# Kernel tuning notes

Measured on AMD Instinct MI355X. Metric: run time of the kernel, lower is better.

The kernel has to match this reference:

```python
import math
import jax, jax.numpy as jnp
import numpy as np

NUM_HEADS = 16
HEAD_DIM = 64
NB_FEATURES = 256
EPS = 1e-06
DATA_NORM = HEAD_DIM ** (-0.25)


def setup_inputs() -> dict:
    key = jax.random.key(0)
    ks = jax.random.split(key, 5)
    B, N, C = 4, 4096, 1024
    x = jax.random.normal(ks[0], (B, N, C), dtype=jnp.float32)
    w_qkv = jax.random.normal(ks[1], (C, 3 * C), dtype=jnp.float32) * (C ** -0.5)
    b_qkv = jnp.zeros((3 * C,), dtype=jnp.float32)
    w_out = jax.random.normal(ks[2], (C, C), dtype=jnp.float32) * (C ** -0.5)
    b_out = jnp.zeros((C,), dtype=jnp.float32)
    proj = jax.random.normal(ks[3], (NUM_HEADS, NB_FEATURES, HEAD_DIM), dtype=jnp.float32)
    proj = proj / jnp.linalg.norm(proj, axis=-1, keepdims=True)  # F.normalize(dim=-1)
    return {"x": x, "w_qkv": w_qkv, "b_qkv": b_qkv, "w_out": w_out, "b_out": b_out,
            "proj_matrix": proj}


def _feature_map(x, proj):
    # x: [b,h,n,d], proj: [h,m,d] -> [b,h,n,m]
    x = x * DATA_NORM
    x_proj = jnp.einsum('bhnd,hmd->bhnm', x, proj)
    sq_norms = 0.5 * jnp.sum(x * x, axis=-1, keepdims=True)
    x_proj = x_proj - sq_norms
    x_proj = x_proj - jnp.max(x_proj, axis=-1, keepdims=True)
    return (jnp.exp(x_proj) + EPS) / math.sqrt(NB_FEATURES)


def reference(x, w_qkv, b_qkv, w_out, b_out, proj_matrix):
    B, N, C = x.shape
    h, d = NUM_HEADS, HEAD_DIM
    qkv = x @ w_qkv + b_qkv                     # [B,N,3C]
    q, k, v = jnp.split(qkv, 3, axis=-1)
    to_heads = lambda z: z.reshape(B, N, h, d).transpose(0, 2, 1, 3)  # [B,h,N,d]
    q, k, v = to_heads(q), to_heads(k), to_heads(v)

    q_prime = _feature_map(q, proj_matrix)      # [B,h,N,m]
    k_prime = _feature_map(k, proj_matrix)      # [B,h,N,m]

    k_sum = jnp.sum(k_prime, axis=2)                          # [B,h,m]
    kv = jnp.einsum('bhnm,bhnd->bhmd', k_prime, v)            # [B,h,m,d]
    numerator = jnp.einsum('bhnm,bhmd->bhnd', q_prime, kv)    # [B,h,N,d]
    denominator = jnp.einsum('bhnm,bhm->bhn', q_prime, k_sum) + EPS
    out = numerator / denominator[..., None]

    out = out.transpose(0, 2, 1, 3).reshape(B, N, C)
    return out @ w_out + b_out
```

## Files before the change

kernel.cpp:

```cpp
#include <hip/hip_runtime.h>
#include <hip/hip_bf16.h>
#include <stdint.h>


#define DN 0.35355339059327379f
#define EPSF 1e-6f
#define INV_SQRT_M 0.0625f

typedef __attribute__((ext_vector_type(8))) short bf16x8;
typedef __attribute__((ext_vector_type(4))) float f32x4;

static __device__ __forceinline__ short f2bf(float f) {
    __hip_bfloat16 h = __float2bfloat16(f);
    return *(short*)&h;
}
static __device__ __forceinline__ void gload16(const void* g, void* l) {
    __builtin_amdgcn_global_load_lds(
        (const __attribute__((address_space(1))) void*)g,
        (__attribute__((address_space(3))) void*)l,
        16, 0, 0);
}

__global__ __launch_bounds__(256) void conv_x(const float* __restrict__ X,
                                              short* __restrict__ Xb) {
    int i = blockIdx.x * 256 + threadIdx.x;
    float4 v = ((const float4*)X)[i];
    short4 o;
    o.x = f2bf(v.x); o.y = f2bf(v.y); o.z = f2bf(v.z); o.w = f2bf(v.w);
    ((short4*)Xb)[i] = o;
}

__global__ __launch_bounds__(256) void convt_w(const float* __restrict__ W,
                                               short* __restrict__ WT,
                                               int K, int NN) {
    __shared__ short tile[64][66];
    int t = threadIdx.x;
    int k0 = blockIdx.y * 64, n0 = blockIdx.x * 64;
    for (int i = t; i < 4096; i += 256) {
        int r = i >> 6, c = i & 63;
        tile[r][c] = f2bf(W[(size_t)(k0 + r) * NN + n0 + c]);
    }
    __syncthreads();
    for (int i = t; i < 4096; i += 256) {
        int r = i >> 6, c = i & 63;
        WT[(size_t)(n0 + r) * K + k0 + c] = tile[c][r];
    }
}

__global__ __launch_bounds__(256) void conv_proj(const float* __restrict__ proj,
                                                 short* __restrict__ pjb) {
    int e = blockIdx.x * 256 + threadIdx.x;
    int m = (e >> 6) & 255, d = e & 63;
    int base = e & ~63;
    pjb[base + (d ^ ((m & 7) << 3))] = f2bf(proj[e]);
}

__global__ __launch_bounds__(256) void mfma_gemm_qkv(const short* __restrict__ A,
                                                     const short* __restrict__ BT,
                                                     const float* __restrict__ bias,
                                                     short* __restrict__ Qh,
                                                     short* __restrict__ Kh,
                                                     short* __restrict__ Vt) {
    const int K = 1024;
    __shared__ short lA[128 * 32];
    __shared__ short lB[128 * 32];
    int t = threadIdx.x, lane = t & 63, w = t >> 6;
    int wm = w >> 1, wn = w & 1;
    int rowBase = blockIdx.y * 128, colBase = blockIdx.x * 128;

    int rs = (lane >> 2), cb = (lane & 3) * 16;
    const char* gA0 = (const char*)(A + (size_t)(rowBase + w * 32 + rs) * K) + cb;
    const char* gA1 = (const char*)(A + (size_t)(rowBase + w * 32 + 16 + rs) * K) + cb;
    const char* gB0 = (const char*)(BT + (size_t)(colBase + w * 32 + rs) * K) + cb;
    const char* gB1 = (const char*)(BT + (size_t)(colBase + w * 32 + 16 + rs) * K) + cb;
    char* dA0 = (char*)lA + (w * 32) * 64;
    char* dA1 = (char*)lA + (w * 32 + 16) * 64;
    char* dB0 = (char*)lB + (w * 32) * 64;
    char* dB1 = (char*)lB + (w * 32 + 16) * 64;

    int offA[4], offB[4];
#pragma unroll
    for (int m = 0; m < 4; ++m) {
        offA[m] = (wm * 64 + m * 16 + (lane & 15)) * 64 + (lane >> 4) * 16;
        offB[m] = (wn * 64 + m * 16 + (lane & 15)) * 64 + (lane >> 4) * 16;
    }

    f32x4 acc[4][4];
#pragma unroll
    for (int m = 0; m < 4; ++m)
#pragma unroll
        for (int n = 0; n < 4; ++n) acc[m][n] = (f32x4){0.f, 0.f, 0.f, 0.f};

    for (int k0 = 0; k0 < K; k0 += 32) {
        size_t kb = (size_t)k0 * 2;
        gload16(gA0 + kb, dA0);
        gload16(gA1 + kb, dA1);
        gload16(gB0 + kb, dB0);
        gload16(gB1 + kb, dB1);
        __syncthreads();
        bf16x8 af[4], bfr[4];
#pragma unroll
        for (int m = 0; m < 4; ++m) af[m] = *(const bf16x8*)((const char*)lA + offA[m]);
#pragma unroll
        for (int n = 0; n < 4; ++n) bfr[n] = *(const bf16x8*)((const char*)lB + offB[n]);
#pragma unroll
        for (int m = 0; m < 4; ++m)
#pragma unroll
            for (int n = 0; n < 4; ++n)
                acc[m][n] = __builtin_amdgcn_mfma_f32_16x16x32_bf16(af[m], bfr[n], acc[m][n], 0, 0, 0);
        __syncthreads();
    }

    int li = lane & 15, g = lane >> 4;
    float bcol[4];
#pragma unroll
    for (int n = 0; n < 4; ++n)
        bcol[n] = bias[colBase + wn * 64 + n * 16 + li];
#pragma unroll
    for (int n = 0; n < 4; ++n) {
        int gc = colBase + wn * 64 + n * 16 + li;
        int which = gc >> 10, cc = gc & 1023, hh = cc >> 6, dd = cc & 63;
        if (which == 2) {
#pragma unroll
            for (int m = 0; m < 4; ++m) {
                int gr0 = rowBase + wm * 64 + m * 16 + g * 4;
                int b = gr0 >> 12, nn0 = gr0 & 4095;
                short4 o;
                o.x = f2bf(acc[m][n][0] + bcol[n]);
                o.y = f2bf(acc[m][n][1] + bcol[n]);
                o.z = f2bf(acc[m][n][2] + bcol[n]);
                o.w = f2bf(acc[m][n][3] + bcol[n]);
                int nsw = (nn0 & ~63) | ((nn0 & 63) ^ ((dd & 7) << 3));
                *(short4*)&Vt[((size_t)(b * 16 + hh) * 64 + dd) * 4096 + nsw] = o;
            }
        } else {
            short* dst = (which == 0) ? Qh : Kh;
#pragma unroll
            for (int m = 0; m < 4; ++m) {
#pragma unroll
                for (int j = 0; j < 4; ++j) {
                    int gr = rowBase + wm * 64 + m * 16 + g * 4 + j;
                    int b = gr >> 12, nn = gr & 4095;
                    int dsw = dd ^ ((nn & 7) << 3);
                    dst[((size_t)(b * 16 + hh) * 4096 + nn) * 64 + dsw] =
                        f2bf((acc[m][n][j] + bcol[n]) * DN);
                }
            }
        }
    }
}

__global__ __launch_bounds__(256) void mfma_gemm_out(const short* __restrict__ A,
                                                     const short* __restrict__ BT,
                                                     const float* __restrict__ bias,
                                                     float* __restrict__ C) {
    const int K = 1024, NN = 1024;
    __shared__ short lA[128 * 32];
    __shared__ short lB[128 * 32];
    int t = threadIdx.x, lane = t & 63, w = t >> 6;
    int wm = w >> 1, wn = w & 1;
    int rowBase = blockIdx.y * 128, colBase = blockIdx.x * 128;

    int rs = (lane >> 2), cb = (lane & 3) * 16;
    const char* gA0 = (const char*)(A + (size_t)(rowBase + w * 32 + rs) * K) + cb;
    const char* gA1 = (const char*)(A + (size_t)(rowBase + w * 32 + 16 + rs) * K) + cb;
    const char* gB0 = (const char*)(BT + (size_t)(colBase + w * 32 + rs) * K) + cb;
    const char* gB1 = (const char*)(BT + (size_t)(colBase + w * 32 + 16 + rs) * K) + cb;
    char* dA0 = (char*)lA + (w * 32) * 64;
    char* dA1 = (char*)lA + (w * 32 + 16) * 64;
    char* dB0 = (char*)lB + (w * 32) * 64;
    char* dB1 = (char*)lB + (w * 32 + 16) * 64;

    int offA[4], offB[4];
#pragma unroll
    for (int m = 0; m < 4; ++m) {
        offA[m] = (wm * 64 + m * 16 + (lane & 15)) * 64 + (lane >> 4) * 16;
        offB[m] = (wn * 64 + m * 16 + (lane & 15)) * 64 + (lane >> 4) * 16;
    }

    f32x4 acc[4][4];
#pragma unroll
    for (int m = 0; m < 4; ++m)
#pragma unroll
        for (int n = 0; n < 4; ++n) acc[m][n] = (f32x4){0.f, 0.f, 0.f, 0.f};

    for (int k0 = 0; k0 < K; k0 += 32) {
        size_t kb = (size_t)k0 * 2;
        gload16(gA0 + kb, dA0);
        gload16(gA1 + kb, dA1);
        gload16(gB0 + kb, dB0);
        gload16(gB1 + kb, dB1);
        __syncthreads();
        bf16x8 af[4], bfr[4];
#pragma unroll
        for (int m = 0; m < 4; ++m) af[m] = *(const bf16x8*)((const char*)lA + offA[m]);
#pragma unroll
        for (int n = 0; n < 4; ++n) bfr[n] = *(const bf16x8*)((const char*)lB + offB[n]);
#pragma unroll
        for (int m = 0; m < 4; ++m)
#pragma unroll
            for (int n = 0; n < 4; ++n)
                acc[m][n] = __builtin_amdgcn_mfma_f32_16x16x32_bf16(af[m], bfr[n], acc[m][n], 0, 0, 0);
        __syncthreads();
    }

    float bcol[4];
#pragma unroll
    for (int n = 0; n < 4; ++n)
        bcol[n] = bias[colBase + wn * 64 + n * 16 + (lane & 15)];
#pragma unroll
    for (int m = 0; m < 4; ++m) {
#pragma unroll
        for (int j = 0; j < 4; ++j) {
            int gr = rowBase + wm * 64 + m * 16 + (lane >> 4) * 4 + j;
#pragma unroll
            for (int n = 0; n < 4; ++n) {
                int gc = colBase + wn * 64 + n * 16 + (lane & 15);
                C[(size_t)gr * NN + gc] = acc[m][n][j] + bcol[n];
            }
        }
    }
}

__global__ __launch_bounds__(256) void fmap_mfma(const short* __restrict__ Kh,
                                                 const short* __restrict__ Vt,
                                                 const short* __restrict__ pjb,
                                                 float* __restrict__ kvpart,
                                                 float* __restrict__ kspart) {
    int bh = blockIdx.y, ch = blockIdx.x, h = bh & 15;
    int t = threadIdx.x, lane = t & 63, w = t >> 6;
    int g = lane >> 4, li = lane & 15;
    __shared__ __align__(16) short pj[256 * 64];
    __shared__ __align__(16) short kt[64 * 64];
    __shared__ __align__(16) short vt[64 * 64];
    __shared__ __align__(16) short Pl[4][64 * 40];
    __shared__ __align__(16) float maxw[4][64];

    {
        const short* psrc = pjb + (size_t)h * 16384;
#pragma unroll
        for (int c2 = 0; c2 < 8; ++c2) {
            int c = 8 * w + c2;
            gload16(psrc + c * 512 + lane * 8, pj + c * 512);
        }
    }

    f32x4 acc[4][4];
#pragma unroll
    for (int i = 0; i < 4; ++i)
#pragma unroll
        for (int j = 0; j < 4; ++j) acc[i][j] = (f32x4){0.f, 0.f, 0.f, 0.f};
    float ksacc[4] = {0.f, 0.f, 0.f, 0.f};

    const short* kbase = Kh + ((size_t)bh * 4096 + ch * 512) * 64;
    const short* vbase = Vt + (size_t)bh * 64 * 4096 + ch * 512;
    int swz = (li & 7) << 4;

    for (int tile = 0; tile < 8; ++tile) {
        __syncthreads();
#pragma unroll
        for (int c2 = 0; c2 < 2; ++c2) {
            int c = 2 * w + c2;
            gload16(kbase + (size_t)(tile * 64) * 64 + c * 512 + lane * 8,
                    kt + c * 512);
            int d = 8 * c + (lane >> 3);
            gload16(vbase + (size_t)d * 4096 + tile * 64 + (lane & 7) * 8,
                    vt + c * 512);
        }
        __syncthreads();

        f32x4 sacc[4][4];
#pragma unroll
        for (int i = 0; i < 4; ++i)
#pragma unroll
            for (int j = 0; j < 4; ++j) sacc[i][j] = (f32x4){0.f, 0.f, 0.f, 0.f};
#pragma unroll
        for (int ks = 0; ks < 2; ++ks) {
            int kb = ks * 64 + g * 16;
            bf16x8 afr[4], bfr[4];
#pragma unroll
            for (int ni = 0; ni < 4; ++ni)
                afr[ni] = *(const bf16x8*)((const char*)kt +
                           (16 * ni + li) * 128 + (kb ^ swz));
#pragma unroll
            for (int mi = 0; mi < 4; ++mi)
                bfr[mi] = *(const bf16x8*)((const char*)pj +
                           (64 * w + 16 * mi + li) * 128 + (kb ^ swz));
#pragma unroll
            for (int ni = 0; ni < 4; ++ni)
#pragma unroll
                for (int mi = 0; mi < 4; ++mi)
                    sacc[ni][mi] = __builtin_amdgcn_mfma_f32_16x16x32_bf16(
                        afr[ni], bfr[mi], sacc[ni][mi], 0, 0, 0);
        }

        float mxl[4][4];
#pragma unroll
        for (int ni = 0; ni < 4; ++ni)
#pragma unroll
            for (int jj = 0; jj < 4; ++jj) {
                float m0 = fmaxf(sacc[ni][0][jj], sacc[ni][1][jj]);
                float m1 = fmaxf(sacc[ni][2][jj], sacc[ni][3][jj]);
                mxl[ni][jj] = fmaxf(m0, m1);
            }
#pragma unroll
        for (int off = 1; off <= 8; off <<= 1)
#pragma unroll
            for (int ni = 0; ni < 4; ++ni)
#pragma unroll
                for (int jj = 0; jj < 4; ++jj)
                    mxl[ni][jj] = fmaxf(mxl[ni][jj], __shfl_xor(mxl[ni][jj], off));
        if (li == 0) {
#pragma unroll
            for (int ni = 0; ni < 4; ++ni)
                *(float4*)&maxw[w][16 * ni + 4 * g] =
                    make_float4(mxl[ni][0], mxl[ni][1], mxl[ni][2], mxl[ni][3]);
        }
        __syncthreads();

#pragma unroll
        for (int hf = 0; hf < 2; ++hf) {
#pragma unroll
            for (int ni2 = 0; ni2 < 2; ++ni2) {
                int ni = 2 * hf + ni2;
                float4 a0 = *(const float4*)&maxw[0][16 * ni + 4 * g];
                float4 a1 = *(const float4*)&maxw[1][16 * ni + 4 * g];
                float4 a2 = *(const float4*)&maxw[2][16 * ni + 4 * g];
                float4 a3 = *(const float4*)&maxw[3][16 * ni + 4 * g];
                float mm[4];
                mm[0] = fmaxf(fmaxf(a0.x, a1.x), fmaxf(a2.x, a3.x));
                mm[1] = fmaxf(fmaxf(a0.y, a1.y), fmaxf(a2.y, a3.y));
                mm[2] = fmaxf(fmaxf(a0.z, a1.z), fmaxf(a2.z, a3.z));
                mm[3] = fmaxf(fmaxf(a0.w, a1.w), fmaxf(a2.w, a3.w));
#pragma unroll
                for (int mi = 0; mi < 4; ++mi) {
                    float p0 = (__expf(sacc[ni][mi][0] - mm[0]) + EPSF) * INV_SQRT_M;
                    float p1 = (__expf(sacc[ni][mi][1] - mm[1]) + EPSF) * INV_SQRT_M;
                    float p2 = (__expf(sacc[ni][mi][2] - mm[2]) + EPSF) * INV_SQRT_M;
                    float p3 = (__expf(sacc[ni][mi][3] - mm[3]) + EPSF) * INV_SQRT_M;
                    ksacc[mi] += (p0 + p1) + (p2 + p3);
                    uint32_t u0 = (uint32_t)(uint16_t)f2bf(p0) |
                                  ((uint32_t)(uint16_t)f2bf(p1) << 16);
                    uint32_t u1 = (uint32_t)(uint16_t)f2bf(p2) |
                                  ((uint32_t)(uint16_t)f2bf(p3) << 16);
                    int m_l = 16 * mi + li;
                    *(uint2*)((char*)Pl[w] + m_l * 80 + 32 * ni2 + 8 * g) =
                        make_uint2(u0, u1);
                }
            }
#pragma unroll
            for (int mi = 0; mi < 4; ++mi) {
                bf16x8 pa = *(const bf16x8*)((const char*)Pl[w] +
                             (16 * mi + li) * 80 + 16 * g);
#pragma unroll
                for (int di = 0; di < 4; ++di) {
                    bf16x8 bv = *(const bf16x8*)((const char*)vt +
                                 (16 * di + li) * 128 + ((64 * hf + 16 * g) ^ swz));
                    acc[mi][di] = __builtin_amdgcn_mfma_f32_16x16x32_bf16(
                        pa, bv, acc[mi][di], 0, 0, 0);
                }
            }
        }
    }

#pragma unroll
    for (int mi = 0; mi < 4; ++mi) {
        ksacc[mi] += __shfl_xor(ksacc[mi], 16);
        ksacc[mi] += __shfl_xor(ksacc[mi], 32);
    }
    if (lane < 16) {
#pragma unroll
        for (int mi = 0; mi < 4; ++mi)
            kspart[(bh * 8 + ch) * 256 + 64 * w + 16 * mi + li] = ksacc[mi];
    }
    float* kvb = kvpart + (size_t)(bh * 8 + ch) * 16384;
#pragma unroll
    for (int mi = 0; mi < 4; ++mi)
#pragma unroll
        for (int di = 0; di < 4; ++di) {
            int d = 16 * di + li, m0 = 64 * w + 16 * mi + 4 * g;
            *(float4*)&kvb[d * 256 + m0] =
                make_float4(acc[mi][di][0], acc[mi][di][1],
                            acc[mi][di][2], acc[mi][di][3]);
        }
}

__global__ __launch_bounds__(256) void reduce_kv(const float* __restrict__ kvpart,
                                                 const float* __restrict__ kspart,
                                                 short* __restrict__ kvsT) {
    int bh = blockIdx.y, bx = blockIdx.x, t = threadIdx.x;
    if (bx < 4) {
#pragma unroll
        for (int i = 0; i < 16; ++i) {
            int idx = t + i * 256;
            int d = 16 * bx + (idx >> 8), m = idx & 255;
            float s = 0.f;
            size_t base = ((size_t)(bh * 8) * 64 + d) * 256 + m;
#pragma unroll
            for (int c = 0; c < 8; ++c) s += kvpart[base + (size_t)c * 16384];
            int widx = (m & 128) + ((m & 127) ^ ((d & 7) << 3));
            kvsT[((size_t)bh * 80 + d) * 256 + widx] = f2bf(s);
        }
    } else {
        float s = 0.f;
#pragma unroll
        for (int c = 0; c < 8; ++c) s += kspart[((bh * 8 + c) << 8) + t];
        kvsT[((size_t)bh * 80 + 64) * 256 + t] = f2bf(s);
        for (int i = t; i < 15 * 256; i += 256) {
            int r = 65 + (i >> 8), cc = i & 255;
            kvsT[((size_t)bh * 80 + r) * 256 + cc] = 0;
        }
    }
}

__global__ __launch_bounds__(256) void contract_mfma(
        const short* __restrict__ Qh,
        const short* __restrict__ pjb,
        const short* __restrict__ kvsT,
        short* __restrict__ attn) {
    int bh = blockIdx.y, rb = blockIdx.x, h = bh & 15, b = bh >> 4;
    int t = threadIdx.x, lane = t & 63, w = t >> 6;
    __shared__ __align__(16) short qs[64 * 64];
    __shared__ __align__(16) short pj[128 * 64];
    __shared__ __align__(16) short Pl[64 * 128];
    __shared__ __align__(16) short kvl[80 * 128];

    {
        const short* src = Qh + ((size_t)bh * 4096 + rb * 64) * 64;
#pragma unroll
        for (int c2 = 0; c2 < 2; ++c2) {
            int c = 2 * w + c2;
            gload16(src + (c * 8 + (lane >> 3)) * 64 + (lane & 7) * 8,
                    qs + c * 512);
        }
    }

    f32x4 acc5[5];
#pragma unroll
    for (int i = 0; i < 5; ++i) acc5[i] = (f32x4){0.f, 0.f, 0.f, 0.f};

    int g = lane >> 4, li = lane & 15;

    for (int half = 0; half < 2; ++half) {
        __syncthreads();
        const short* psrc = pjb + (size_t)h * 16384 + half * 8192;
#pragma unroll
        for (int c2 = 0; c2 < 4; ++c2) {
            int c = 4 * w + c2;
            gload16(psrc + (c * 8 + (lane >> 3)) * 64 + (lane & 7) * 8,
                    pj + c * 512);
        }
        const short* ksrc = kvsT + (size_t)bh * 80 * 256 + half * 128;
#pragma unroll
        for (int c2 = 0; c2 < 5; ++c2) {
            int c = 5 * w + c2;
            gload16(ksrc + (c * 4 + (lane >> 4)) * 256 + (lane & 15) * 8,
                    kvl + c * 512);
        }
        __syncthreads();

        f32x4 sacc[2][4];
#pragma unroll
        for (int mi = 0; mi < 2; ++mi)
#pragma unroll
            for (int ni = 0; ni < 4; ++ni) sacc[mi][ni] = (f32x4){0.f, 0.f, 0.f, 0.f};
#pragma unroll
        for (int ks = 0; ks < 2; ++ks) {
            int kbyte = ks * 64 + g * 16;
            bf16x8 afr[2], bfr[4];
#pragma unroll
            for (int mi = 0; mi < 2; ++mi) {
                int mr = 32 * w + 16 * mi + li;
                afr[mi] = *(const bf16x8*)((const char*)pj +
                           mr * 128 + (kbyte ^ ((mr & 7) << 4)));
            }
#pragma unroll
            for (int ni = 0; ni < 4; ++ni) {
                int qr = 16 * ni + li;
                bfr[ni] = *(const bf16x8*)((const char*)qs +
                           qr * 128 + (kbyte ^ ((qr & 7) << 4)));
            }
#pragma unroll
            for (int mi = 0; mi < 2; ++mi)
#pragma unroll
                for (int ni = 0; ni < 4; ++ni)
                    sacc[mi][ni] = __builtin_amdgcn_mfma_f32_16x16x32_bf16(
                        afr[mi], bfr[ni], sacc[mi][ni], 0, 0, 0);
        }

#pragma unroll
        for (int mi = 0; mi < 2; ++mi) {
            int m0 = 32 * w + 16 * mi + 4 * g;
#pragma unroll
            for (int ni = 0; ni < 4; ++ni) {
                int row = 16 * ni + li;
                float e0 = (__expf(sacc[mi][ni][0]) + EPSF) * INV_SQRT_M;
                float e1 = (__expf(sacc[mi][ni][1]) + EPSF) * INV_SQRT_M;
                float e2 = (__expf(sacc[mi][ni][2]) + EPSF) * INV_SQRT_M;
                float e3 = (__expf(sacc[mi][ni][3]) + EPSF) * INV_SQRT_M;
                uint32_t u0 = (uint32_t)(uint16_t)f2bf(e0) |
                              ((uint32_t)(uint16_t)f2bf(e1) << 16);
                uint32_t u1 = (uint32_t)(uint16_t)f2bf(e2) |
                              ((uint32_t)(uint16_t)f2bf(e3) << 16);
                int byte = row * 256 + ((m0 * 2) ^ ((row & 7) << 4));
                *(uint2*)((char*)Pl + byte) = make_uint2(u0, u1);
            }
        }
        __syncthreads();

        int rowA = 16 * w + li;
        int abase = rowA * 256;
        int asw = (rowA & 7) << 4;
#pragma unroll
        for (int ks = 0; ks < 4; ++ks) {
            int kbyte = ks * 64 + g * 16;
            bf16x8 pa = *(const bf16x8*)((const char*)Pl + abase + (kbyte ^ asw));
#pragma unroll
            for (int ni = 0; ni < 5; ++ni) {
                int rowB = 16 * ni + li;
                bf16x8 bv = *(const bf16x8*)((const char*)kvl +
                             rowB * 256 + (kbyte ^ ((rowB & 7) << 4)));
                acc5[ni] = __builtin_amdgcn_mfma_f32_16x16x32_bf16(
                    pa, bv, acc5[ni], 0, 0, 0);
            }
        }
    }

    float dj[4];
#pragma unroll
    for (int jj = 0; jj < 4; ++jj)
        dj[jj] = __shfl(acc5[4][jj], lane & 48) + EPSF;
#pragma unroll
    for (int ni = 0; ni < 4; ++ni) {
        int d = 16 * ni + li;
#pragma unroll
        for (int jj = 0; jj < 4; ++jj) {
            int n = rb * 64 + 16 * w + 4 * g + jj;
            attn[((size_t)b * 4096 + n) * 1024 + h * 64 + d] =
                f2bf(acc5[ni][jj] / dj[jj]);
        }
    }
}

extern "C" void kernel_launch(void* const* d_in, const int* in_sizes, int n_in,
                              void* d_out, int out_size, void* d_ws, size_t ws_size,
                              hipStream_t stream) {
    const float* x      = (const float*)d_in[0];
    const float* w_qkv  = (const float*)d_in[1];
    const float* b_qkv  = (const float*)d_in[2];
    const float* w_out  = (const float*)d_in[3];
    const float* b_out  = (const float*)d_in[4];
    const float* proj   = (const float*)d_in[5];
    float* out = (float*)d_out;

    char* w = (char*)d_ws;
    short* xb     = (short*)(w);
    short* wqT    = (short*)(w + 33554432);
    short* wOT    = (short*)(w + 39845888);
    short* Qh     = (short*)(w + 41943040);
    short* Kh     = (short*)(w + 75497472);
    short* Vt     = (short*)(w + 109051904);
    float* kvpart = (float*)(w);
    float* kspart = (float*)(w + 142606336);
    short* kvsT   = (short*)(w + 143130624);
    short* pjb    = (short*)(w + 145752064);
    short* attn   = Kh;

    conv_x<<<dim3(16384), 256, 0, stream>>>(x, xb);
    convt_w<<<dim3(48, 16), 256, 0, stream>>>(w_qkv, wqT, 1024, 3072);
    convt_w<<<dim3(16, 16), 256, 0, stream>>>(w_out, wOT, 1024, 1024);
    conv_proj<<<dim3(1024), 256, 0, stream>>>(proj, pjb);
    mfma_gemm_qkv<<<dim3(24, 128), 256, 0, stream>>>(xb, wqT, b_qkv, Qh, Kh, Vt);
    fmap_mfma<<<dim3(8, 64), 256, 0, stream>>>(Kh, Vt, pjb, kvpart, kspart);
    reduce_kv<<<dim3(5, 64), 256, 0, stream>>>(kvpart, kspart, kvsT);
    contract_mfma<<<dim3(64, 64), 256, 0, stream>>>(Qh, pjb, kvsT, attn);
    mfma_gemm_out<<<dim3(8, 128), 256, 0, stream>>>(attn, wOT, b_out, out);
}
```

Baseline: 341.6 us.

## Double-buffer GEMM K-loop with swizzled LDS, block remapping, and staged epilogue stores

Both projection GEMMs now share one core that stages 64-wide K tiles into two LDS buffers with an XOR swizzle. The next tile's loads are issued before computing the current one, so fewer barriers are needed and global latency overlaps the MFMA work. The 1D grid is remapped so neighbouring blocks share operand rows and columns for better L2 reuse. Epilogues stage results through LDS so Q/K and the output are written with wide vector stores instead of scattered scalar ones, at the cost of 64KB LDS per block, which may limit occupancy.

```diff
diff --git a/kernel.cpp b/kernel.cpp
--- a/kernel.cpp
+++ b/kernel.cpp
@@ -55,72 +55,105 @@
     pjb[base + (d ^ ((m & 7) << 3))] = f2bf(proj[e]);
 }
 
-__global__ __launch_bounds__(256) void mfma_gemm_qkv(const short* __restrict__ A,
-                                                     const short* __restrict__ BT,
-                                                     const float* __restrict__ bias,
-                                                     short* __restrict__ Qh,
-                                                     short* __restrict__ Kh,
-                                                     short* __restrict__ Vt) {
+__device__ __forceinline__ void gemm_core128(const short* __restrict__ A,
+                                             const short* __restrict__ BT,
+                                             int rowBase, int colBase,
+                                             char* smem, f32x4 acc[4][4]) {
     const int K = 1024;
-    __shared__ short lA[128 * 32];
-    __shared__ short lB[128 * 32];
     int t = threadIdx.x, lane = t & 63, w = t >> 6;
+    int li = lane & 15, g = lane >> 4;
     int wm = w >> 1, wn = w & 1;
-    int rowBase = blockIdx.y * 128, colBase = blockIdx.x * 128;
-
-    int rs = (lane >> 2), cb = (lane & 3) * 16;
-    const char* gA0 = (const char*)(A + (size_t)(rowBase + w * 32 + rs) * K) + cb;
-    const char* gA1 = (const char*)(A + (size_t)(rowBase + w * 32 + 16 + rs) * K) + cb;
-    const char* gB0 = (const char*)(BT + (size_t)(colBase + w * 32 + rs) * K) + cb;
-    const char* gB1 = (const char*)(BT + (size_t)(colBase + w * 32 + 16 + rs) * K) + cb;
-    char* dA0 = (char*)lA + (w * 32) * 64;
-    char* dA1 = (char*)lA + (w * 32 + 16) * 64;
-    char* dB0 = (char*)lB + (w * 32) * 64;
-    char* dB1 = (char*)lB + (w * 32 + 16) * 64;
-
-    int offA[4], offB[4];
-#pragma unroll
-    for (int m = 0; m < 4; ++m) {
-        offA[m] = (wm * 64 + m * 16 + (lane & 15)) * 64 + (lane >> 4) * 16;
-        offB[m] = (wn * 64 + m * 16 + (lane & 15)) * 64 + (lane >> 4) * 16;
-    }
+
+    const char* aSrc[4]; const char* bSrc[4]; int aOff[4];
+#pragma unroll
+    for (int c = 0; c < 4; ++c) {
+        int idx = c * 256 + t;
+        int r = idx >> 3, s = t & 7;
+        aOff[c] = idx * 16;
+        aSrc[c] = (const char*)(A + (size_t)(rowBase + r) * K + ((s ^ (r & 7)) * 8));
+        bSrc[c] = (const char*)(BT + (size_t)(colBase + r) * K + ((s ^ (r & 7)) * 8));
+    }
+#pragma unroll
+    for (int m = 0; m < 4; ++m)
+#pragma unroll
+        for (int n = 0; n < 4; ++n) acc[m][n] = (f32x4){0.f, 0.f, 0.f, 0.f};
+
+#pragma unroll
+    for (int c = 0; c < 4; ++c) {
+        gload16(aSrc[c], smem + aOff[c]);
+        gload16(bSrc[c], smem + 16384 + aOff[c]);
+    }
+
+    int swz = (li & 7) << 4;
+
+    for (int tt = 0; tt < 16; ++tt) {
+        int cur = tt & 1;
+        if (tt < 15) {
+            char* d = smem + (cur ^ 1) * 32768;
+#pragma unroll
+            for (int c = 0; c < 4; ++c) {
+                gload16(aSrc[c] + (size_t)(tt + 1) * 128, d + aOff[c]);
+                gload16(bSrc[c] + (size_t)(tt + 1) * 128, d + 16384 + aOff[c]);
+            }
+            asm volatile("s_waitcnt vmcnt(8)" ::: "memory");
+        } else {
+            asm volatile("s_waitcnt vmcnt(0)" ::: "memory");
+        }
+        __builtin_amdgcn_sched_barrier(0);
+        __builtin_amdgcn_s_barrier();
+        __builtin_amdgcn_sched_barrier(0);
+        __builtin_amdgcn_s_setprio(1);
+        const char* bA = smem + cur * 32768;
+        const char* bB = bA + 16384;
+#pragma unroll
+        for (int ks = 0; ks < 2; ++ks) {
+            int kb = ks * 64 + g * 16;
+            bf16x8 af[4], bv[4];
+#pragma unroll
+            for (int m = 0; m < 4; ++m)
+                af[m] = *(const bf16x8*)(bA + (wm * 64 + m * 16 + li) * 128 + (kb ^ swz));
+#pragma unroll
+            for (int n = 0; n < 4; ++n)
+                bv[n] = *(const bf16x8*)(bB + (wn * 64 + n * 16 + li) * 128 + (kb ^ swz));
+#pragma unroll
+            for (int m = 0; m < 4; ++m)
+#pragma unroll
+                for (int n = 0; n < 4; ++n)
+                    acc[m][n] = __builtin_amdgcn_mfma_f32_16x16x32_bf16(
+                        af[m], bv[n], acc[m][n], 0, 0, 0);
+        }
+        __builtin_amdgcn_s_setprio(0);
+        __builtin_amdgcn_sched_barrier(0);
+        __builtin_amdgcn_s_barrier();
+        __builtin_amdgcn_sched_barrier(0);
+    }
+}
+
+__global__ __launch_bounds__(256, 2) void mfma_gemm_qkv(
+        const short* __restrict__ A, const short* __restrict__ BT,
+        const float* __restrict__ bias,
+        short* __restrict__ Qh, short* __restrict__ Kh, short* __restrict__ Vt) {
+    __shared__ __align__(16) char smem[65536];
+    int t = threadIdx.x, lane = t & 63, w = t >> 6;
+    int li = lane & 15, g = lane >> 4, wm = w >> 1, wn = w & 1;
+    int lin = blockIdx.x;
+    int sz = (lin & 7) * 384 + (lin >> 3);
+    int bx = sz % 24, by = sz / 24;
+    int rowBase = by * 128, colBase = bx * 128;
 
     f32x4 acc[4][4];
-#pragma unroll
-    for (int m = 0; m < 4; ++m)
-#pragma unroll
-        for (int n = 0; n < 4; ++n) acc[m][n] = (f32x4){0.f, 0.f, 0.f, 0.f};
-
-    for (int k0 = 0; k0 < K; k0 += 32) {
-        size_t kb = (size_t)k0 * 2;
-        gload16(gA0 + kb, dA0);
-        gload16(gA1 + kb, dA1);
-        gload16(gB0 + kb, dB0);
-        gload16(gB1 + kb, dB1);
-        __syncthreads();
-        bf16x8 af[4], bfr[4];
-#pragma unroll
-        for (int m = 0; m < 4; ++m) af[m] = *(const bf16x8*)((const char*)lA + offA[m]);
-#pragma unroll
-        for (int n = 0; n < 4; ++n) bfr[n] = *(const bf16x8*)((const char*)lB + offB[n]);
-#pragma unroll
-        for (int m = 0; m < 4; ++m)
-#pragma unroll
-            for (int n = 0; n < 4; ++n)
-                acc[m][n] = __builtin_amdgcn_mfma_f32_16x16x32_bf16(af[m], bfr[n], acc[m][n], 0, 0, 0);
-        __syncthreads();
-    }
-
-    int li = lane & 15, g = lane >> 4;
+    gemm_core128(A, BT, rowBase, colBase, smem, acc);
+
     float bcol[4];
 #pragma unroll
-    for (int n = 0; n < 4; ++n)
-        bcol[n] = bias[colBase + wn * 64 + n * 16 + li];
-#pragma unroll
-    for (int n = 0; n < 4; ++n) {
-        int gc = colBase + wn * 64 + n * 16 + li;
-        int which = gc >> 10, cc = gc & 1023, hh = cc >> 6, dd = cc & 63;
-        if (which == 2) {
+    for (int n = 0; n < 4; ++n) bcol[n] = bias[colBase + wn * 64 + n * 16 + li];
+    int whichB = colBase >> 10;
+
+    if (whichB == 2) {
+#pragma unroll
+        for (int n = 0; n < 4; ++n) {
+            int gc = colBase + wn * 64 + n * 16 + li;
+            int hh = (gc & 1023) >> 6, dd = gc & 63;
 #pragma unroll
             for (int m = 0; m < 4; ++m) {
                 int gr0 = rowBase + wm * 64 + m * 16 + g * 4;
@@ -133,92 +166,75 @@
                 int nsw = (nn0 & ~63) | ((nn0 & 63) ^ ((dd & 7) << 3));
                 *(short4*)&Vt[((size_t)(b * 16 + hh) * 64 + dd) * 4096 + nsw] = o;
             }
-        } else {
-            short* dst = (which == 0) ? Qh : Kh;
-#pragma unroll
-            for (int m = 0; m < 4; ++m) {
-#pragma unroll
-                for (int j = 0; j < 4; ++j) {
-                    int gr = rowBase + wm * 64 + m * 16 + g * 4 + j;
-                    int b = gr >> 12, nn = gr & 4095;
-                    int dsw = dd ^ ((nn & 7) << 3);
-                    dst[((size_t)(b * 16 + hh) * 4096 + nn) * 64 + dsw] =
-                        f2bf((acc[m][n][j] + bcol[n]) * DN);
-                }
-            }
-        }
-    }
-}
-
-__global__ __launch_bounds__(256) void mfma_gemm_out(const short* __restrict__ A,
-                                                     const short* __restrict__ BT,
-                                                     const float* __restrict__ bias,
-                                                     float* __restrict__ C) {
-    const int K = 1024, NN = 1024;
-    __shared__ short lA[128 * 32];
-    __shared__ short lB[128 * 32];
+        }
+    } else {
+        short* dst = (whichB == 0) ? Qh : Kh;
+        int hh = ((colBase + wn * 64) & 1023) >> 6;
+        float* wreg = (float*)(smem + w * 8704);
+#pragma unroll
+        for (int r = 0; r < 2; ++r) {
+#pragma unroll
+            for (int mi = 0; mi < 2; ++mi)
+#pragma unroll
+                for (int n = 0; n < 4; ++n)
+#pragma unroll
+                    for (int jj = 0; jj < 4; ++jj)
+                        wreg[(mi * 16 + g * 4 + jj) * 68 + n * 16 + li] =
+                            (acc[2 * r + mi][n][jj] + bcol[n]) * DN;
+            int row = lane >> 1, h2 = lane & 1;
+            int tok = rowBase + wm * 64 + r * 32 + row;
+            int b = tok >> 12, nn = tok & 4095;
+            size_t base = ((size_t)(b * 16 + hh) * 4096 + nn) * 64;
+#pragma unroll
+            for (int k = 0; k < 4; ++k) {
+                float4 v0 = *(const float4*)&wreg[row * 68 + h2 * 32 + k * 8];
+                float4 v1 = *(const float4*)&wreg[row * 68 + h2 * 32 + k * 8 + 4];
+                bf16x8 ov;
+                ov[0] = f2bf(v0.x); ov[1] = f2bf(v0.y);
+                ov[2] = f2bf(v0.z); ov[3] = f2bf(v0.w);
+                ov[4] = f2bf(v1.x); ov[5] = f2bf(v1.y);
+                ov[6] = f2bf(v1.z); ov[7] = f2bf(v1.w);
+                int dgrp = (h2 * 4 + k) ^ (tok & 7);
+                *(bf16x8*)&dst[base + dgrp * 8] = ov;
+            }
+        }
+    }
+}
+
+__global__ __launch_bounds__(256, 2) void mfma_gemm_out(
+        const short* __restrict__ A, const short* __restrict__ BT,
+        const float* __restrict__ bias, float* __restrict__ C) {
+    __shared__ __align__(16) char smem[65536];
     int t = threadIdx.x, lane = t & 63, w = t >> 6;
-    int wm = w >> 1, wn = w & 1;
-    int rowBase = blockIdx.y * 128, colBase = blockIdx.x * 128;
-
-    int rs = (lane >> 2), cb = (lane & 3) * 16;
-    const char* gA0 = (const char*)(A + (size_t)(rowBase + w * 32 + rs) * K) + cb;
-    const char* gA1 = (const char*)(A + (size_t)(rowBase + w * 32 + 16 + rs) * K) + cb;
-    const char* gB0 = (const char*)(BT + (size_t)(colBase + w * 32 + rs) * K) + cb;
-    const char* gB1 = (const char*)(BT + (size_t)(colBase + w * 32 + 16 + rs) * K) + cb;
-    char* dA0 = (char*)lA + (w * 32) * 64;
-    char* dA1 = (char*)lA + (w * 32 + 16) * 64;
-    char* dB0 = (char*)lB + (w * 32) * 64;
-    char* dB1 = (char*)lB + (w * 32 + 16) * 64;
-
-    int offA[4], offB[4];
-#pragma unroll
-    for (int m = 0; m < 4; ++m) {
-        offA[m] = (wm * 64 + m * 16 + (lane & 15)) * 64 + (lane >> 4) * 16;
-        offB[m] = (wn * 64 + m * 16 + (lane & 15)) * 64 + (lane >> 4) * 16;
-    }
+    int li = lane & 15, g = lane >> 4, wm = w >> 1, wn = w & 1;
+    int lin = blockIdx.x;
+    int sz = (lin & 7) * 128 + (lin >> 3);
+    int bx = sz & 7, by = sz >> 3;
+    int rowBase = by * 128, colBase = bx * 128;
 
     f32x4 acc[4][4];
-#pragma unroll
-    for (int m = 0; m < 4; ++m)
-#pragma unroll
-        for (int n = 0; n < 4; ++n) acc[m][n] = (f32x4){0.f, 0.f, 0.f, 0.f};
-
-    for (int k0 = 0; k0 < K; k0 += 32) {
-        size_t kb = (size_t)k0 * 2;
-        gload16(gA0 + kb, dA0);
-        gload16(gA1 + kb, dA1);
-        gload16(gB0 + kb, dB0);
-        gload16(gB1 + kb, dB1);
-        __syncthreads();
-        bf16x8 af[4], bfr[4];
-#pragma unroll
-        for (int m = 0; m < 4; ++m) af[m] = *(const bf16x8*)((const char*)lA + offA[m]);
-#pragma unroll
-        for (int n = 0; n < 4; ++n) bfr[n] = *(const bf16x8*)((const char*)lB + offB[n]);
-#pragma unroll
-        for (int m = 0; m < 4; ++m)
+    gemm_core128(A, BT, rowBase, colBase, smem, acc);
+
+    float bcol[4];
+#pragma unroll
+    for (int n = 0; n < 4; ++n) bcol[n] = bias[colBase + wn * 64 + n * 16 + li];
+    float* wreg = (float*)(smem + w * 8704);
+#pragma unroll
+    for (int r = 0; r < 2; ++r) {
+#pragma unroll
+        for (int mi = 0; mi < 2; ++mi)
 #pragma unroll
             for (int n = 0; n < 4; ++n)
-                acc[m][n] = __builtin_amdgcn_mfma_f32_16x16x32_bf16(af[m], bfr[n], acc[m][n], 0, 0, 0);
-        __syncthreads();
-    }
-
-    float bcol[4];
-#pragma unroll
-    for (int n = 0; n < 4; ++n)
-        bcol[n] = bias[colBase + wn * 64 + n * 16 + (lane & 15)];
-#pragma unroll
-    for (int m = 0; m < 4; ++m) {
-#pragma unroll
-        for (int j = 0; j < 4; ++j) {
-            int gr = rowBase + wm * 64 + m * 16 + (lane >> 4) * 4 + j;
-#pragma unroll
-            for (int n = 0; n < 4; ++n) {
-                int gc = colBase + wn * 64 + n * 16 + (lane & 15);
-                C[(size_t)gr * NN + gc] = acc[m][n][j] + bcol[n];
-            }
-        }
+#pragma unroll
+                for (int jj = 0; jj < 4; ++jj)
+                    wreg[(mi * 16 + g * 4 + jj) * 68 + n * 16 + li] =
+                        acc[2 * r + mi][n][jj] + bcol[n];
+        int row = lane >> 1, h2 = lane & 1;
+        int gr = rowBase + wm * 64 + r * 32 + row;
+        float* cp = C + (size_t)gr * 1024 + colBase + wn * 64 + h2 * 32;
+#pragma unroll
+        for (int k = 0; k < 8; ++k)
+            *(float4*)&cp[k * 4] = *(const float4*)&wreg[row * 68 + h2 * 32 + k * 4];
     }
 }
 
@@ -570,9 +586,9 @@
     convt_w<<<dim3(48, 16), 256, 0, stream>>>(w_qkv, wqT, 1024, 3072);
     convt_w<<<dim3(16, 16), 256, 0, stream>>>(w_out, wOT, 1024, 1024);
     conv_proj<<<dim3(1024), 256, 0, stream>>>(proj, pjb);
-    mfma_gemm_qkv<<<dim3(24, 128), 256, 0, stream>>>(xb, wqT, b_qkv, Qh, Kh, Vt);
+    mfma_gemm_qkv<<<dim3(3072), 256, 0, stream>>>(xb, wqT, b_qkv, Qh, Kh, Vt);
     fmap_mfma<<<dim3(8, 64), 256, 0, stream>>>(Kh, Vt, pjb, kvpart, kspart);
     reduce_kv<<<dim3(5, 64), 256, 0, stream>>>(kvpart, kspart, kvsT);
     contract_mfma<<<dim3(64, 64), 256, 0, stream>>>(Qh, pjb, kvsT, attn);
-    mfma_gemm_out<<<dim3(8, 128), 256, 0, stream>>>(attn, wOT, b_out, out);
-}
+    mfma_gemm_out<<<dim3(1024), 256, 0, stream>>>(attn, wOT, b_out, out);
+}
```

Result: faster. 333.3 us (-2.4%).
